# Performance work log

Measured on AMD Instinct MI355X. Metric: run time of the kernel, lower is better.

The kernel has to match this reference:

```python
import jax, jax.numpy as jnp
import numpy as np

DIM = 128      # input node feature dim
GS = 64        # SAGEConv output dim
AF = 32        # additional (ir_score) feature dim
NB = 2         # nb_classes
G = 8192       # num_graphs in batch
NPG = 16       # nodes per graph
N = G * NPG    # total nodes = 131072
E = 2097152    # total edges (avg degree 16)


def setup_inputs() -> dict:
    key = jax.random.key(0)
    ks = jax.random.split(key, 10)

    def w(k, shape, fan_in):
        return jax.random.normal(k, shape, jnp.float32) / np.sqrt(fan_in)

    return {
        "x": jax.random.normal(ks[0], (N, DIM), jnp.float32),
        "edge_index": jax.random.randint(ks[1], (2, E), 0, N),
        "set_indices": jax.random.randint(ks[2], (G, 2), 0, NPG),
        "batch_ids": jnp.repeat(jnp.arange(G), NPG),  # sorted graph ids, PyG style
        "ir_score": jax.random.uniform(ks[3], (G, AF), jnp.float32),
        "W_l": w(ks[4], (DIM, GS), DIM),
        "b_l": jnp.zeros((GS,), jnp.float32),
        "W_r": w(ks[5], (DIM, GS), DIM),
        "W_ir": w(ks[6], (AF, 2 * GS), AF),
        "b_ir": jnp.zeros((2 * GS,), jnp.float32),
        "W1": w(ks[7], ((2 * GS) * (2 * GS), 200), (2 * GS) * (2 * GS)),
        "b1": jnp.zeros((200,), jnp.float32),
        "W2": w(ks[8], (200, NB), 200),
        "b2": jnp.zeros((NB,), jnp.float32),
    }


def reference(x, edge_index, set_indices, batch_ids, ir_score,
              W_l, b_l, W_r, W_ir, b_ir, W1, b1, W2, b2):
    n = x.shape[0]
    src, dst = edge_index[0], edge_index[1]

    # SAGEConv (mean aggregation): out = lin_l(mean_{j in N(i)} x_j) + lin_r(x_i)
    agg = jax.ops.segment_sum(x[src], dst, num_segments=n)           # [N, DIM]
    deg = jax.ops.segment_sum(jnp.ones((src.shape[0],), x.dtype), dst, num_segments=n)
    mean = agg / jnp.maximum(deg, 1.0)[:, None]
    h = jax.nn.relu(mean @ W_l + b_l + x @ W_r)                      # [N, GS]

    # per-graph node counts -> index bases (cumsum), then global pair indices
    g = set_indices.shape[0]
    num_nodes = jax.ops.segment_sum(jnp.ones((n,), jnp.float32), batch_ids, num_segments=g)
    csum = jnp.cumsum(num_nodes.astype(jnp.int64))
    index_bases = jnp.concatenate([jnp.zeros((1,), jnp.int64), csum[:-1]])
    sib = index_bases[:, None] + set_indices                         # [G, 2]

    pair = h[sib].reshape(g, 2 * GS)                                 # gather + flatten

    # fusion: relu(linear(ir_score)) then per-graph outer product
    S = jax.nn.relu(ir_score @ W_ir + b_ir)                          # [G, 2*GS]
    outer = jnp.einsum('gi,gj->gij', pair, S).reshape(g, -1)         # [G, (2GS)^2]

    # decode MLP
    z = jax.nn.relu(outer @ W1 + b1)                                 # [G, 200]
    logits = z @ W2 + b2                                             # [G, NB]
    return logits
```

## Files before the change

kernel.cpp:

```cpp
#include <hip/hip_runtime.h>

#define NN   131072
#define GG   8192
#define EE   2097152
#define KBIG 16384
#define NPAD 208
#define NSPLIT 8
#define NSEL  16384
#define SBUCK 256
#define SUBC  4
#define SCAPS 336
#define SCAPT (SUBC*SCAPS)

typedef _Float16 half_t;
typedef __attribute__((ext_vector_type(8))) _Float16 half8;
typedef __attribute__((ext_vector_type(4))) float floatx4;

__device__ inline floatx4 mfma16(half8 a, half8 b, floatx4 c) {
  return __builtin_amdgcn_mfma_f32_16x16x32_f16(a, b, c, 0, 0, 0);
}

__global__ void prep_w(const float* __restrict__ Wl, const float* __restrict__ Wr,
                       half_t* __restrict__ Wt) {
  int idx = blockIdx.x * blockDim.x + threadIdx.x;
  int n = idx >> 7, k = idx & 127;
  float v = (n < 64) ? Wl[k * 64 + n] : Wr[k * 64 + (n - 64)];
  Wt[n * 128 + k] = (half_t)v;
}
__global__ void prep_w1p(const float* __restrict__ W1, half_t* __restrict__ W1p) {
  int idx = blockIdx.x * blockDim.x + threadIdx.x;
  int lane = idx & 63;
  int t = idx >> 6;
  int nt = t % 13; t /= 13;
  int jc = t & 3;  t >>= 2;
  int i  = t & 15; t >>= 4;
  int split = t;
  int n = nt * 16 + (lane & 15);
  int k0 = split * 2048 + i * 128 + jc * 32 + (lane >> 4) * 8;
  half8 v;
#pragma unroll
  for (int e = 0; e < 8; e++)
    v[e] = (half_t)((n < 200) ? W1[(size_t)(k0 + e) * 200 + n] : 0.f);
  *(half8*)(W1p + (size_t)idx * 8) = v;
}

__global__ void set_slots(const int* __restrict__ set_idx, int* __restrict__ nodemap,
                          int* __restrict__ slot_node) {
  int idx = blockIdx.x * blockDim.x + threadIdx.x;
  int g = idx >> 1, which = idx & 1;
  int node = g * 16 + set_idx[g * 2 + which];
  slot_node[idx] = node;
  nodemap[node] = idx;
}

__global__ void filter_scatter(const int* __restrict__ src, const int* __restrict__ dst,
                               const int* __restrict__ nodemap,
                               int* __restrict__ scnt, unsigned int* __restrict__ sbuf) {
  int e = blockIdx.x * blockDim.x + threadIdx.x;
  int d = dst[e];
  int slot = nodemap[d];
  if (slot >= 0) {
    int b = slot >> 6;
    int sub = blockIdx.x & (SUBC - 1);
    int pos = atomicAdd(&scnt[(b * SUBC + sub) * 16], 1);
    if (pos < SCAPS)
      sbuf[(size_t)(b * SUBC + sub) * SCAPS + pos] =
          (unsigned int)src[e] | ((unsigned int)(slot & 63) << 17);
  }
}

__global__ __launch_bounds__(256) void y_gemm(const float* __restrict__ x,
                                              const half_t* __restrict__ WtG,
                                              half_t* __restrict__ y16) {
  __shared__ half_t wlds[64 * 128];
  __shared__ half_t ybuf[64 * 72];
  int tid = threadIdx.x, w = tid >> 6, lane = tid & 63;
  int m = lane & 15, q = lane >> 4, kc = q * 8;
#pragma unroll
  for (int it = 0; it < 4; it++) {
    int cb = (it * 4 + w) * 64;
    const half_t* g = WtG + ((size_t)cb + lane) * 8;
    half_t* l = wlds + (size_t)cb * 8;
    __builtin_amdgcn_global_load_lds((const __attribute__((address_space(1))) uint32_t*)g,
                                     (__attribute__((address_space(3))) uint32_t*)l, 16, 0, 0);
  }
  int node0 = blockIdx.x * 64 + w * 16;
  float4 xu[4][2];
#pragma unroll
  for (int step = 0; step < 4; step++) {
    const float* xp = x + (size_t)(node0 + m) * 128 + step * 32 + kc;
    xu[step][0] = *(const float4*)xp;
    xu[step][1] = *(const float4*)(xp + 4);
  }
  __syncthreads();
  floatx4 acc[4];
#pragma unroll
  for (int nt = 0; nt < 4; nt++) acc[nt] = (floatx4){0.f, 0.f, 0.f, 0.f};
#pragma unroll
  for (int step = 0; step < 4; step++) {
    float4 u0 = xu[step][0], u1 = xu[step][1];
    half8 av = {(half_t)u0.x, (half_t)u0.y, (half_t)u0.z, (half_t)u0.w,
                (half_t)u1.x, (half_t)u1.y, (half_t)u1.z, (half_t)u1.w};
    int k0 = step * 32 + kc;
#pragma unroll
    for (int nt = 0; nt < 4; nt++) {
      half8 bv = *(const half8*)(wlds + (nt * 16 + m) * 128 + k0);
      acc[nt] = mfma16(av, bv, acc[nt]);
    }
  }
#pragma unroll
  for (int nt = 0; nt < 4; nt++)
#pragma unroll
    for (int r = 0; r < 4; r++)
      ybuf[(w * 16 + q * 4 + r) * 72 + nt * 16 + m] = (half_t)acc[nt][r];
  __syncthreads();
#pragma unroll
  for (int c = tid; c < 512; c += 256) {
    int row = c >> 3, co = (c & 7) * 8;
    *(half8*)(y16 + (size_t)(blockIdx.x * 64 + row) * 64 + co) =
        *(const half8*)(ybuf + row * 72 + co);
  }
}

__global__ __launch_bounds__(256) void r_slots(const float* __restrict__ x,
                                               const half_t* __restrict__ WtG,
                                               const float* __restrict__ b_l,
                                               const int* __restrict__ slot_node,
                                               half_t* __restrict__ r_slot) {
  int tid = threadIdx.x, w = tid >> 6, lane = tid & 63;
  int m = lane & 15, q = lane >> 4, kc = q * 8;
  int s0 = blockIdx.x * 64 + w * 16;
  int node = slot_node[s0 + m];
  floatx4 acc[4];
#pragma unroll
  for (int nt = 0; nt < 4; nt++) acc[nt] = (floatx4){0.f, 0.f, 0.f, 0.f};
#pragma unroll
  for (int step = 0; step < 4; step++) {
    int k0 = step * 32 + kc;
    const float* xp = x + (size_t)node * 128 + k0;
    float4 u0 = *(const float4*)xp;
    float4 u1 = *(const float4*)(xp + 4);
    half8 av = {(half_t)u0.x, (half_t)u0.y, (half_t)u0.z, (half_t)u0.w,
                (half_t)u1.x, (half_t)u1.y, (half_t)u1.z, (half_t)u1.w};
#pragma unroll
    for (int nt = 0; nt < 4; nt++) {
      half8 bv = *(const half8*)(WtG + (size_t)(64 + nt * 16 + m) * 128 + k0);
      acc[nt] = mfma16(av, bv, acc[nt]);
    }
  }
#pragma unroll
  for (int nt = 0; nt < 4; nt++) {
    int n = nt * 16 + m;
    float bias = b_l[n];
#pragma unroll
    for (int r = 0; r < 4; r++) {
      int s = s0 + q * 4 + r;
      r_slot[(size_t)s * 64 + n] = (half_t)(acc[nt][r] + bias);
    }
  }
}

__global__ __launch_bounds__(256) void slot_agg(const unsigned int* __restrict__ sbuf,
                                                const int* __restrict__ scnt,
                                                const half_t* __restrict__ y16,
                                                const half_t* __restrict__ r_slot,
                                                half_t* __restrict__ h_slot) {
  __shared__ int sorted[SCAPT];
  __shared__ int hist[64];
  __shared__ int base[64];
  __shared__ int start[65];
  int b = blockIdx.x, tid = threadIdx.x;
  if (tid < 64) hist[tid] = 0;
  __syncthreads();
  unsigned int myedge[2 * SUBC];
  int mycnt = 0;
#pragma unroll
  for (int sub = 0; sub < SUBC; sub++) {
    int n = scnt[(b * SUBC + sub) * 16]; if (n > SCAPS) n = SCAPS;
    const unsigned int* eb = sbuf + (size_t)(b * SUBC + sub) * SCAPS;
    for (int e = tid; e < n; e += 256) {
      unsigned int pk = eb[e];
      myedge[mycnt++] = pk;
      atomicAdd(&hist[pk >> 17], 1);
    }
  }
  __syncthreads();
  if (tid < 64) {
    int v = hist[tid];
    int sum = v;
#pragma unroll
    for (int off = 1; off < 64; off <<= 1) {
      int u = __shfl_up(sum, off);
      if (tid >= off) sum += u;
    }
    start[tid] = sum - v;
    base[tid]  = sum - v;
    if (tid == 63) start[64] = sum;
  }
  __syncthreads();
  for (int i = 0; i < mycnt; i++) {
    unsigned int pk = myedge[i];
    int pos = atomicAdd(&base[pk >> 17], 1);
    sorted[pos] = (int)(pk & 0x1FFFF);
  }
  __syncthreads();
  int s = tid >> 2, p = tid & 3;
  int e0 = start[s], e1 = start[s + 1];
  float acc[16];
#pragma unroll
  for (int j = 0; j < 16; j++) acc[j] = 0.f;
  int e = e0;
  for (; e + 2 <= e1; e += 2) {
    int s0 = sorted[e], s1 = sorted[e + 1];
    const half8* p0 = (const half8*)(y16 + (size_t)s0 * 64 + p * 16);
    const half8* p1 = (const half8*)(y16 + (size_t)s1 * 64 + p * 16);
    half8 a0 = p0[0], c0 = p0[1], a1 = p1[0], c1 = p1[1];
#pragma unroll
    for (int j = 0; j < 8; j++) {
      acc[j]     += (float)a0[j] + (float)a1[j];
      acc[8 + j] += (float)c0[j] + (float)c1[j];
    }
  }
  if (e < e1) {
    int s0 = sorted[e];
    const half8* p0 = (const half8*)(y16 + (size_t)s0 * 64 + p * 16);
    half8 a0 = p0[0], c0 = p0[1];
#pragma unroll
    for (int j = 0; j < 8; j++) { acc[j] += (float)a0[j]; acc[8 + j] += (float)c0[j]; }
  }
  int slot = b * 64 + s;
  float inv = 1.0f / fmaxf((float)(e1 - e0), 1.0f);
  const half8* rr = (const half8*)(r_slot + (size_t)slot * 64 + p * 16);
  half8 r0 = rr[0], r1 = rr[1];
  half8 o0, o1;
#pragma unroll
  for (int j = 0; j < 8; j++) {
    o0[j] = (half_t)fmaxf(acc[j] * inv + (float)r0[j], 0.f);
    o1[j] = (half_t)fmaxf(acc[8 + j] * inv + (float)r1[j], 0.f);
  }
  half8* hp = (half8*)(h_slot + (size_t)slot * 64 + p * 16);
  hp[0] = o0;
  hp[1] = o1;
}

__global__ void s_pair_kernel(const float* __restrict__ ir, const float* __restrict__ W_ir,
                              const float* __restrict__ b_ir, half_t* __restrict__ S16,
                              const half_t* __restrict__ h_slot,
                              const int* __restrict__ nodemap,
                              const int* __restrict__ set_idx, half_t* __restrict__ pair16) {
  int idx = blockIdx.x * blockDim.x + threadIdx.x;
  int g = idx >> 7, o = idx & 127;
  const float* irow = ir + g * 32;
  float sv = b_ir[o];
#pragma unroll
  for (int a = 0; a < 32; a++) sv += irow[a] * W_ir[a * 128 + o];
  S16[idx] = (half_t)fmaxf(sv, 0.f);
  int which = o >> 6, c = o & 63;
  int node = g * 16 + set_idx[g * 2 + which];
  int slot = nodemap[node];
  pair16[idx] = h_slot[(size_t)slot * 64 + c];
}

__global__ __launch_bounds__(256, 2) void biggemm(const half_t* __restrict__ pair16,
                                                  const half_t* __restrict__ S16,
                                                  const half_t* __restrict__ W1p,
                                                  float* __restrict__ zpart) {
  __shared__ half_t bbuf[2][26 * 512];
  __shared__ half_t pls[16][128];
  int bx = blockIdx.x;
  int mt = bx >> 3, split = bx & 7;
  int g0 = mt * 128;
  int tid = threadIdx.x, w = tid >> 6, lane = tid & 63;
  int m = lane & 15, q = lane >> 4, kc = q * 8;

  auto stage = [&](int ii, int halfsel, int bufsel) {
#pragma unroll
    for (int ff = 0; ff < 7; ff++) {
      int f = ff * 4 + w;
      if (f < 26) {
        const half_t* gsrc = W1p + (((size_t)(split * 16 + ii) * 52) + halfsel * 26 + f) * 512 + lane * 8;
        half_t* ldst = &bbuf[bufsel][f * 512];
        __builtin_amdgcn_global_load_lds((const __attribute__((address_space(1))) uint32_t*)gsrc,
                                         (__attribute__((address_space(3))) uint32_t*)ldst, 16, 0, 0);
      }
    }
  };

  stage(0, 0, 0);

  {
    int row = tid & 127, sel = tid >> 7;
    half8 pa = *(const half8*)(pair16 + (size_t)(g0 + row) * 128 + split * 16 + sel * 8);
#pragma unroll
    for (int j = 0; j < 8; j++) pls[sel * 8 + j][row] = pa[j];
  }

  half8 sf[2][4];
#pragma unroll
  for (int sub = 0; sub < 2; sub++) {
    int grow = g0 + w * 32 + sub * 16 + m;
#pragma unroll
    for (int jc = 0; jc < 4; jc++)
      sf[sub][jc] = *(const half8*)(S16 + (size_t)grow * 128 + jc * 32 + kc);
  }

  floatx4 acc[2][13];
#pragma unroll
  for (int sb = 0; sb < 2; sb++)
#pragma unroll
    for (int nt = 0; nt < 13; nt++) acc[sb][nt] = (floatx4){0.f, 0.f, 0.f, 0.f};

  for (int i = 0; i < 16; i++) {
    half_t p0, p1;
#pragma unroll
    for (int h2 = 0; h2 < 2; h2++) {
      __syncthreads();
      if (h2 == 0) {
        p0 = pls[i][w * 32 + 0 * 16 + m];
        p1 = pls[i][w * 32 + 1 * 16 + m];
        stage(i, 1, 1);
      } else if (i < 15) {
        stage(i + 1, 0, 0);
      }
      const half_t* bb = bbuf[h2];
#pragma unroll
      for (int jj = 0; jj < 2; jj++) {
        const int jc = h2 * 2 + jj;
        half8 a0 = sf[0][jc] * p0;
        half8 a1 = sf[1][jc] * p1;
#pragma unroll
        for (int nt = 0; nt < 13; nt++) {
          half8 bv = *(const half8*)(bb + (jj * 13 + nt) * 512 + lane * 8);
          acc[0][nt] = mfma16(a0, bv, acc[0][nt]);
          acc[1][nt] = mfma16(a1, bv, acc[1][nt]);
        }
      }
    }
  }

#pragma unroll
  for (int sub = 0; sub < 2; sub++)
#pragma unroll
    for (int nt = 0; nt < 13; nt++)
#pragma unroll
      for (int r = 0; r < 4; r++) {
        int row = g0 + w * 32 + sub * 16 + q * 4 + r;
        zpart[((size_t)split * GG + row) * NPAD + nt * 16 + m] = acc[sub][nt][r];
      }
}

__global__ __launch_bounds__(256) void reduce_mlp(const float* __restrict__ zpart,
                                                  const float* __restrict__ b1,
                                                  const float* __restrict__ W2,
                                                  const float* __restrict__ b2,
                                                  float* __restrict__ out) {
  int tid = threadIdx.x;
  int w = tid >> 6, lane = tid & 63;
  int g = blockIdx.x * 4 + w;
  float p0 = 0.f, p1 = 0.f;
#pragma unroll
  for (int qq = 0; qq < 4; qq++) {
    int c = qq * 64 + lane;
    if (c < 200) {
      float z = 0.f;
#pragma unroll
      for (int sp = 0; sp < NSPLIT; sp++)
        z += zpart[((size_t)sp * GG + g) * NPAD + c];
      z += b1[c];
      z = fmaxf(z, 0.f);
      p0 += z * W2[c * 2];
      p1 += z * W2[c * 2 + 1];
    }
  }
#pragma unroll
  for (int off = 32; off; off >>= 1) {
    p0 += __shfl_down(p0, off);
    p1 += __shfl_down(p1, off);
  }
  if (lane == 0) {
    out[g * 2] = p0 + b2[0];
    out[g * 2 + 1] = p1 + b2[1];
  }
}

extern "C" void kernel_launch(void* const* d_in, const int* in_sizes, int n_in,
                              void* d_out, int out_size, void* d_ws, size_t ws_size,
                              hipStream_t stream) {
  const float* x     = (const float*)d_in[0];
  const int*   ei    = (const int*)d_in[1];
  const int*   setix = (const int*)d_in[2];
  const float* ir    = (const float*)d_in[4];
  const float* W_l   = (const float*)d_in[5];
  const float* b_l   = (const float*)d_in[6];
  const float* W_r   = (const float*)d_in[7];
  const float* W_ir  = (const float*)d_in[8];
  const float* b_ir  = (const float*)d_in[9];
  const float* W1    = (const float*)d_in[10];
  const float* b1    = (const float*)d_in[11];
  const float* W2    = (const float*)d_in[12];
  const float* b2    = (const float*)d_in[13];
  float* out = (float*)d_out;

  char* ws = (char*)d_ws;
  size_t off = 0;
  auto alloc = [&](size_t bytes) -> void* {
    void* p = ws + off;
    off = (off + bytes + 255) & ~(size_t)255;
    return p;
  };
  size_t pool_start = off;
  int* nodemap   = (int*)alloc((size_t)NN * 4);
  int* slot_node = (int*)alloc((size_t)NSEL * 4);
  int* scnt      = (int*)alloc((size_t)SBUCK * SUBC * 16 * 4);
  unsigned int* sbuf = (unsigned int*)alloc((size_t)SBUCK * SUBC * SCAPS * 4);
  half_t* y16    = (half_t*)alloc((size_t)NN * 64 * 2);
  half_t* r_slot = (half_t*)alloc((size_t)NSEL * 64 * 2);
  half_t* h_slot = (half_t*)alloc((size_t)NSEL * 64 * 2);
  float* zpart = (float*)(ws + pool_start);
  {
    size_t zend = pool_start + (((size_t)NSPLIT * GG * NPAD * 4 + 255) & ~(size_t)255);
    if (off < zend) off = zend;
  }
  half_t* Wt     = (half_t*)alloc(128 * 128 * 2);
  half_t* W1p    = (half_t*)alloc((size_t)NPAD * KBIG * 2);
  half_t* S16    = (half_t*)alloc((size_t)GG * 128 * 2);
  half_t* pair16 = (half_t*)alloc((size_t)GG * 128 * 2);
  (void)ws_size; (void)in_sizes; (void)n_in; (void)out_size;

  const int* esrc = ei;
  const int* edst = ei + EE;

  hipMemsetAsync(nodemap, 0xFF, (size_t)NN * 4, stream);
  hipMemsetAsync(scnt, 0, (size_t)SBUCK * SUBC * 16 * 4, stream);

  prep_w<<<(128 * 128) / 256, 256, 0, stream>>>(W_l, W_r, Wt);
  prep_w1p<<<(NPAD * KBIG / 8) / 256, 256, 0, stream>>>(W1, W1p);

  set_slots<<<NSEL / 256, 256, 0, stream>>>(setix, nodemap, slot_node);
  filter_scatter<<<EE / 256, 256, 0, stream>>>(esrc, edst, nodemap, scnt, sbuf);

  y_gemm<<<NN / 64, 256, 0, stream>>>(x, Wt, y16);
  r_slots<<<NSEL / 64, 256, 0, stream>>>(x, Wt, b_l, slot_node, r_slot);
  slot_agg<<<SBUCK, 256, 0, stream>>>(sbuf, scnt, y16, r_slot, h_slot);

  s_pair_kernel<<<(GG * 128) / 256, 256, 0, stream>>>(ir, W_ir, b_ir, S16, h_slot, nodemap, setix, pair16);

  biggemm<<<(GG / 128) * NSPLIT, 256, 0, stream>>>(pair16, S16, W1p, zpart);
  reduce_mlp<<<GG / 4, 256, 0, stream>>>(zpart, b1, W2, b2, out);
}
```

Baseline: 257.4 us.

## Retile biggemm waves to 2x2 grid with padded N and LDS-staged epilogue

Result: slower. 303.1 us (+17.8%).

```diff
diff --git a/kernel.cpp b/kernel.cpp
--- a/kernel.cpp
+++ b/kernel.cpp
@@ -4,7 +4,7 @@
 #define GG   8192
 #define EE   2097152
 #define KBIG 16384
-#define NPAD 208
+#define NPAD 224
 #define NSPLIT 8
 #define NSEL  16384
 #define SBUCK 256
@@ -31,7 +31,7 @@
   int idx = blockIdx.x * blockDim.x + threadIdx.x;
   int lane = idx & 63;
   int t = idx >> 6;
-  int nt = t % 13; t /= 13;
+  int nt = t % 14; t /= 14;
   int jc = t & 3;  t >>= 2;
   int i  = t & 15; t >>= 4;
   int split = t;
@@ -265,24 +265,24 @@
                                                   const half_t* __restrict__ S16,
                                                   const half_t* __restrict__ W1p,
                                                   float* __restrict__ zpart) {
-  __shared__ half_t bbuf[2][26 * 512];
+  __shared__ __align__(16) half_t bbuf[2][28 * 512];
   __shared__ half_t pls[16][128];
   int bx = blockIdx.x;
   int mt = bx >> 3, split = bx & 7;
   int g0 = mt * 128;
   int tid = threadIdx.x, w = tid >> 6, lane = tid & 63;
+  int wm = w >> 1, wn = w & 1;
   int m = lane & 15, q = lane >> 4, kc = q * 8;
+  int ntb = wn * 7;
 
   auto stage = [&](int ii, int halfsel, int bufsel) {
 #pragma unroll
     for (int ff = 0; ff < 7; ff++) {
       int f = ff * 4 + w;
-      if (f < 26) {
-        const half_t* gsrc = W1p + (((size_t)(split * 16 + ii) * 52) + halfsel * 26 + f) * 512 + lane * 8;
-        half_t* ldst = &bbuf[bufsel][f * 512];
-        __builtin_amdgcn_global_load_lds((const __attribute__((address_space(1))) uint32_t*)gsrc,
-                                         (__attribute__((address_space(3))) uint32_t*)ldst, 16, 0, 0);
-      }
+      const half_t* gsrc = W1p + (((size_t)(split * 16 + ii) * 56) + halfsel * 28 + f) * 512 + lane * 8;
+      half_t* ldst = &bbuf[bufsel][f * 512];
+      __builtin_amdgcn_global_load_lds((const __attribute__((address_space(1))) uint32_t*)gsrc,
+                                       (__attribute__((address_space(3))) uint32_t*)ldst, 16, 0, 0);
     }
   };
 
@@ -295,29 +295,31 @@
     for (int j = 0; j < 8; j++) pls[sel * 8 + j][row] = pa[j];
   }
 
-  half8 sf[2][4];
-#pragma unroll
-  for (int sub = 0; sub < 2; sub++) {
-    int grow = g0 + w * 32 + sub * 16 + m;
+  half8 sf[4][4];
+#pragma unroll
+  for (int sub = 0; sub < 4; sub++) {
+    int grow = g0 + wm * 64 + sub * 16 + m;
 #pragma unroll
     for (int jc = 0; jc < 4; jc++)
       sf[sub][jc] = *(const half8*)(S16 + (size_t)grow * 128 + jc * 32 + kc);
   }
 
-  floatx4 acc[2][13];
-#pragma unroll
-  for (int sb = 0; sb < 2; sb++)
-#pragma unroll
-    for (int nt = 0; nt < 13; nt++) acc[sb][nt] = (floatx4){0.f, 0.f, 0.f, 0.f};
+  floatx4 acc[4][7];
+#pragma unroll
+  for (int sb = 0; sb < 4; sb++)
+#pragma unroll
+    for (int t = 0; t < 7; t++) acc[sb][t] = (floatx4){0.f, 0.f, 0.f, 0.f};
 
   for (int i = 0; i < 16; i++) {
-    half_t p0, p1;
+    half_t p0, p1, p2, p3;
 #pragma unroll
     for (int h2 = 0; h2 < 2; h2++) {
       __syncthreads();
       if (h2 == 0) {
-        p0 = pls[i][w * 32 + 0 * 16 + m];
-        p1 = pls[i][w * 32 + 1 * 16 + m];
+        p0 = pls[i][wm * 64 + 0 * 16 + m];
+        p1 = pls[i][wm * 64 + 1 * 16 + m];
+        p2 = pls[i][wm * 64 + 2 * 16 + m];
+        p3 = pls[i][wm * 64 + 3 * 16 + m];
         stage(i, 1, 1);
       } else if (i < 15) {
         stage(i + 1, 0, 0);
@@ -328,25 +330,46 @@
         const int jc = h2 * 2 + jj;
         half8 a0 = sf[0][jc] * p0;
         half8 a1 = sf[1][jc] * p1;
-#pragma unroll
-        for (int nt = 0; nt < 13; nt++) {
-          half8 bv = *(const half8*)(bb + (jj * 13 + nt) * 512 + lane * 8);
-          acc[0][nt] = mfma16(a0, bv, acc[0][nt]);
-          acc[1][nt] = mfma16(a1, bv, acc[1][nt]);
+        half8 a2 = sf[2][jc] * p2;
+        half8 a3 = sf[3][jc] * p3;
+#pragma unroll
+        for (int t = 0; t < 7; t++) {
+          half8 bv = *(const half8*)(bb + (jj * 14 + ntb + t) * 512 + lane * 8);
+          acc[0][t] = mfma16(a0, bv, acc[0][t]);
+          acc[1][t] = mfma16(a1, bv, acc[1][t]);
+          acc[2][t] = mfma16(a2, bv, acc[2][t]);
+          acc[3][t] = mfma16(a3, bv, acc[3][t]);
         }
       }
     }
   }
 
-#pragma unroll
-  for (int sub = 0; sub < 2; sub++)
-#pragma unroll
-    for (int nt = 0; nt < 13; nt++)
-#pragma unroll
-      for (int r = 0; r < 4; r++) {
-        int row = g0 + w * 32 + sub * 16 + q * 4 + r;
-        zpart[((size_t)split * GG + row) * NPAD + nt * 16 + m] = acc[sub][nt][r];
+  float* ebuf = (float*)bbuf;
+#pragma unroll
+  for (int c = 0; c < 4; c++) {
+    __syncthreads();
+    if (wm == (c >> 1)) {
+      int sb0 = (c & 1) * 2;
+#pragma unroll
+      for (int ss = 0; ss < 2; ss++) {
+#pragma unroll
+        for (int t = 0; t < 7; t++)
+#pragma unroll
+          for (int r = 0; r < 4; r++) {
+            int lr = ss * 16 + q * 4 + r;
+            ebuf[lr * 228 + (ntb + t) * 16 + m] = acc[sb0 + ss][t][r];
+          }
       }
+    }
+    __syncthreads();
+    int rbase = g0 + (c >> 1) * 64 + (c & 1) * 32;
+#pragma unroll
+    for (int u = tid; u < 1792; u += 256) {
+      int lr = u / 56, co = (u % 56) * 4;
+      *(float4*)(zpart + ((size_t)split * GG + rbase + lr) * NPAD + co) =
+          *(const float4*)(ebuf + lr * 228 + co);
+    }
+  }
 }
 
 __global__ __launch_bounds__(256) void reduce_mlp(const float* __restrict__ zpart,
```
